# Kernel optimization log

Measured on AMD Instinct MI355X. Metric: run time of the kernel, lower is better.

Reference implementation:

```python
import jax, jax.numpy as jnp
import numpy as np

N, T, D, H = 64, 1024, 512, 512

def setup_inputs() -> dict:
    key = jax.random.key(0)
    k1, k2, k3, k4 = jax.random.split(key, 4)
    x = jax.random.normal(k1, (N, T, D), dtype=jnp.float32)
    h0 = jax.random.normal(k2, (N, H), dtype=jnp.float32)
    Wx = jax.random.normal(k3, (D, H), dtype=jnp.float32) / jnp.sqrt(jnp.float32(D))
    Wh = jax.random.normal(k4, (H, H), dtype=jnp.float32) / jnp.sqrt(jnp.float32(H))
    b = jnp.zeros((H,), dtype=jnp.float32)
    return {"x": x, "h0": h0, "Wx": Wx, "Wh": Wh, "b": b}

def reference(x, h0, Wx, Wh, b):
    # Precompute input projection for all timesteps: (N,T,H)
    xW = jnp.einsum('ntd,dh->nth', x, Wx) + b
    # Sequential recurrence over time via lax.scan
    def step(prev_h, xw_t):
        next_h = jnp.tanh(prev_h @ Wh + xw_t)  # (N,H)
        return next_h, next_h
    # scan over time axis: move T to leading axis
    _, h_seq = jax.lax.scan(step, h0, jnp.swapaxes(xW, 0, 1))  # (T,N,H)
    return jnp.swapaxes(h_seq, 0, 1)  # (N,T,H)
```

## Files before the change

### kernel.cpp

```cpp
#include <hip/hip_runtime.h>
#include <hip/hip_fp16.h>
#include <cstddef>
#include <cstdint>

#define NB 64
#define TT 1024
#define DD 512
#define HH 512

typedef _Float16 h2_t __attribute__((ext_vector_type(2)));
typedef __attribute__((ext_vector_type(8))) short bf16x8;
typedef __attribute__((ext_vector_type(4))) float f32x4;
typedef __attribute__((ext_vector_type(8))) unsigned short ushort8;

__device__ __forceinline__ float dot2f(uint32_t a, uint32_t b, float c) {
#if __has_builtin(__builtin_amdgcn_fdot2)
    return __builtin_amdgcn_fdot2(__builtin_bit_cast(h2_t, a),
                                  __builtin_bit_cast(h2_t, b), c, false);
#else
    __half2 av = __builtin_bit_cast(__half2, a);
    __half2 bv = __builtin_bit_cast(__half2, b);
    float2 af = __half22float2(av), bf = __half22float2(bv);
    return fmaf(af.x, bf.x, fmaf(af.y, bf.y, c));
#endif
}

__device__ __forceinline__ float fast_tanh(float z) {
    z = fmaxf(-15.f, fminf(15.f, z));
    float u = __builtin_amdgcn_exp2f(-2.885390082f * z);
    return (1.f - u) * __builtin_amdgcn_rcpf(1.f + u);
}

__device__ __forceinline__ unsigned short f2bf(float f) {
    uint32_t u = __builtin_bit_cast(uint32_t, f);
    u += 0x7FFFu + ((u >> 16) & 1u);
    return (unsigned short)(u >> 16);
}

__global__ void conv_wt(const float* __restrict__ W,
                        unsigned short* __restrict__ Wt) {
    int n = blockIdx.x;
    int kc = threadIdx.x;
    ushort8 o;
#pragma unroll
    for (int i = 0; i < 8; ++i)
        o[i] = f2bf(W[(size_t)(kc * 8 + i) * HH + n]);
    *reinterpret_cast<ushort8*>(&Wt[(size_t)n * DD + kc * 8]) = o;
}

#define GBM 128
#define GBN 128
#define GBK 64
#define LDSW 72

__global__ __launch_bounds__(256, 4) void gemm_bf16f(
    const float* __restrict__ X,
    const unsigned short* __restrict__ Bt,
    const float* __restrict__ bias,
    float* __restrict__ C)
{
    __shared__ unsigned short As[GBM * LDSW];
    __shared__ unsigned short Bs[GBN * LDSW];

    const int tid  = threadIdx.x;
    const int m0   = blockIdx.x * GBM;
    const int n0   = blockIdx.y * GBN;
    const int lane = tid & 63;
    const int wave = tid >> 6;
    const int wm   = wave >> 1;
    const int wn   = wave & 1;

    const int axr = tid >> 1;
    const int axc = (tid & 1) * 32;
    const int srow = tid >> 3;
    const int sch  = tid & 7;

    f32x4 acc[4][4] = {};

    const int arow = wm * 64 + (lane & 15);
    const int brow = wn * 64 + (lane & 15);
    const int koff = (lane >> 4) * 8;

    for (int kt = 0; kt < DD / GBK; ++kt) {
        const int k0 = kt * GBK;
        {
            const float* xp = &X[(size_t)(m0 + axr) * DD + k0 + axc];
#pragma unroll
            for (int i = 0; i < 4; ++i) {
                float4 a = *reinterpret_cast<const float4*>(&xp[i * 8]);
                float4 b = *reinterpret_cast<const float4*>(&xp[i * 8 + 4]);
                ushort8 o;
                o[0] = f2bf(a.x); o[1] = f2bf(a.y);
                o[2] = f2bf(a.z); o[3] = f2bf(a.w);
                o[4] = f2bf(b.x); o[5] = f2bf(b.y);
                o[6] = f2bf(b.z); o[7] = f2bf(b.w);
                *reinterpret_cast<ushort8*>(&As[axr * LDSW + axc + i * 8]) = o;
            }
        }
#pragma unroll
        for (int p = 0; p < 4; ++p) {
            const int row = srow + p * 32;
            *reinterpret_cast<ushort8*>(&Bs[row * LDSW + sch * 8]) =
                *reinterpret_cast<const ushort8*>(
                    &Bt[(size_t)(n0 + row) * DD + k0 + sch * 8]);
        }
        __syncthreads();

#pragma unroll
        for (int kk = 0; kk < GBK; kk += 32) {
            bf16x8 af[4], bf[4];
#pragma unroll
            for (int mt = 0; mt < 4; ++mt)
                af[mt] = *reinterpret_cast<const bf16x8*>(
                    &As[(arow + mt * 16) * LDSW + kk + koff]);
#pragma unroll
            for (int nt = 0; nt < 4; ++nt)
                bf[nt] = *reinterpret_cast<const bf16x8*>(
                    &Bs[(brow + nt * 16) * LDSW + kk + koff]);
#pragma unroll
            for (int mt = 0; mt < 4; ++mt)
#pragma unroll
                for (int nt = 0; nt < 4; ++nt)
                    acc[mt][nt] = __builtin_amdgcn_mfma_f32_16x16x32_bf16(
                        af[mt], bf[nt], acc[mt][nt], 0, 0, 0);
        }
        __syncthreads();
    }

#pragma unroll
    for (int nt = 0; nt < 4; ++nt) {
        const int col = n0 + wn * 64 + nt * 16 + (lane & 15);
        const float bv = bias[col];
#pragma unroll
        for (int mt = 0; mt < 4; ++mt) {
            const int rbase = m0 + wm * 64 + mt * 16 + (lane >> 4) * 4;
#pragma unroll
            for (int r = 0; r < 4; ++r)
                C[(size_t)(rbase + r) * HH + col] = acc[mt][nt][r] + bv;
        }
    }
}

#define BM 128
#define BN 128
#define BK 8

__global__ __launch_bounds__(256, 2) void gemm_xw(
    const float* __restrict__ A,
    const float* __restrict__ B,
    const float* __restrict__ bias,
    float* __restrict__ C)
{
    __shared__ float As[BK][BM];
    __shared__ float Bs[BK][BN];

    const int tid  = threadIdx.x;
    const int tm   = tid >> 4;
    const int tn   = tid & 15;
    const int row0 = blockIdx.x * BM;
    const int col0 = blockIdx.y * BN;

    const int ar = tid >> 1;
    const int ac = (tid & 1) * 4;
    const int br = tid >> 5;
    const int bc = (tid & 31) * 4;

    float acc[8][8];
#pragma unroll
    for (int i = 0; i < 8; ++i)
#pragma unroll
        for (int j = 0; j < 8; ++j) acc[i][j] = 0.f;

    for (int k0 = 0; k0 < DD; k0 += BK) {
        float4 av = *reinterpret_cast<const float4*>(
            &A[(size_t)(row0 + ar) * DD + k0 + ac]);
        float4 bv = *reinterpret_cast<const float4*>(
            &B[(size_t)(k0 + br) * HH + col0 + bc]);

        As[ac + 0][ar] = av.x;
        As[ac + 1][ar] = av.y;
        As[ac + 2][ar] = av.z;
        As[ac + 3][ar] = av.w;
        *reinterpret_cast<float4*>(&Bs[br][bc]) = bv;
        __syncthreads();

#pragma unroll
        for (int kk = 0; kk < BK; ++kk) {
            float a[8], b[8];
            *reinterpret_cast<float4*>(&a[0]) =
                *reinterpret_cast<const float4*>(&As[kk][tm * 8]);
            *reinterpret_cast<float4*>(&a[4]) =
                *reinterpret_cast<const float4*>(&As[kk][tm * 8 + 4]);
            *reinterpret_cast<float4*>(&b[0]) =
                *reinterpret_cast<const float4*>(&Bs[kk][tn * 8]);
            *reinterpret_cast<float4*>(&b[4]) =
                *reinterpret_cast<const float4*>(&Bs[kk][tn * 8 + 4]);
#pragma unroll
            for (int i = 0; i < 8; ++i)
#pragma unroll
                for (int j = 0; j < 8; ++j)
                    acc[i][j] = fmaf(a[i], b[j], acc[i][j]);
        }
        __syncthreads();
    }

#pragma unroll
    for (int i = 0; i < 8; ++i) {
        const int row = row0 + tm * 8 + i;
#pragma unroll
        for (int j = 0; j < 8; j += 4) {
            const int col = col0 + tn * 8 + j;
            float4 o;
            o.x = acc[i][j + 0] + bias[col + 0];
            o.y = acc[i][j + 1] + bias[col + 1];
            o.z = acc[i][j + 2] + bias[col + 2];
            o.w = acc[i][j + 3] + bias[col + 3];
            *reinterpret_cast<float4*>(&C[(size_t)row * HH + col]) = o;
        }
    }
}

__global__ __launch_bounds__(1024, 4) void rnn_scan_pk2(
    const float* __restrict__ Wh,
    const float* __restrict__ h0,
    float* __restrict__ out,
    uint64_t* __restrict__ truth,
    uint64_t* __restrict__ mirror,
    int* __restrict__ meta)
{
    __shared__ __align__(16) uint32_t hp[2][HH / 2];
    __shared__ float partial[16][128];
    __shared__ int sh_batch, sh_role, sh_fast;

    const int tid = threadIdx.x;

    int xcd_raw;
    asm volatile("s_getreg_b32 %0, hwreg(HW_REG_XCC_ID)" : "=s"(xcd_raw));
    const int xcd = xcd_raw & 7;

    if (tid == 0) {
        int pos = __hip_atomic_fetch_add(&meta[xcd], 1, __ATOMIC_RELAXED,
                                         __HIP_MEMORY_SCOPE_AGENT);
        __hip_atomic_fetch_add(&meta[8], 1, __ATOMIC_RELEASE,
                               __HIP_MEMORY_SCOPE_AGENT);
        while (__hip_atomic_load(&meta[8], __ATOMIC_ACQUIRE,
                                 __HIP_MEMORY_SCOPE_AGENT) < 256)
            __builtin_amdgcn_s_sleep(8);
        int c[8];
#pragma unroll
        for (int q = 0; q < 8; ++q)
            c[q] = __hip_atomic_load(&meta[q], __ATOMIC_RELAXED,
                                     __HIP_MEMORY_SCOPE_AGENT);
        int totalfull = 0, basefull = 0, rembase = 0;
#pragma unroll
        for (int q = 0; q < 8; ++q) totalfull += c[q] >> 2;
        for (int q = 0; q < xcd; ++q) {
            basefull += c[q] >> 2;
            rembase  += c[q] & 3;
        }
        const int nf4 = (c[xcd] >> 2) << 2;
        if (pos < nf4) {
            sh_batch = basefull + (pos >> 2);
            sh_role  = pos & 3;
            sh_fast  = 1;
        } else {
            int ridx = rembase + (pos - nf4);
            sh_batch = totalfull + (ridx >> 2);
            sh_role  = ridx & 3;
            sh_fast  = 0;
        }
    }
    __syncthreads();

    const int n    = sh_batch;
    const int jb   = sh_role << 7;
    const int pb   = sh_role << 6;
    const int fast = sh_fast;

    const int w = tid >> 6;
    const int l = tid & 63;

    uint32_t w0[16], w1[16];
    {
        const float* wc = Wh + (size_t)(w * 32) * HH + jb + l;
#pragma unroll
        for (int p = 0; p < 16; ++p) {
            float e0 = wc[(size_t)(2 * p) * HH];
            float e1 = wc[(size_t)(2 * p + 1) * HH];
            w0[p] = __builtin_bit_cast(uint32_t, __floats2half2_rn(e0, e1));
            float f0 = wc[(size_t)(2 * p) * HH + 64];
            float f1 = wc[(size_t)(2 * p + 1) * HH + 64];
            w1[p] = __builtin_bit_cast(uint32_t, __floats2half2_rn(f0, f1));
        }
    }

    if (tid < HH)
        ((__half*)hp[0])[tid] = __float2half(h0[(size_t)n * HH + tid]);
    __syncthreads();

    float* outn = out + (size_t)n * TT * HH;
    uint64_t* tru = truth  + (size_t)n * 2 * 256;
    uint64_t* mir = mirror + (size_t)n * 2 * 256;

    const int ppi = (pb + 64 + (tid - 64)) & 255;

    int cur = 0;
    for (int t = 0; t < TT; ++t) {
        const uint32_t T = (uint32_t)(t + 1);
        const int slot = (int)(T & 1u);

        float2 xw2 = {0.f, 0.f};
        if (tid < 64)
            xw2 = *reinterpret_cast<const float2*>(
                &outn[(size_t)t * HH + jb + 2 * tid]);

        const uint32_t* hpw = &hp[cur][w * 16];
        float a0 = 0.f, a1 = 0.f, b0 = 0.f, b1 = 0.f;
#pragma unroll
        for (int q = 0; q < 4; ++q) {
            uint4 hv = ((const uint4*)hpw)[q];
            a0 = dot2f(hv.x, w0[4 * q + 0], a0);
            b0 = dot2f(hv.x, w1[4 * q + 0], b0);
            a1 = dot2f(hv.y, w0[4 * q + 1], a1);
            b1 = dot2f(hv.y, w1[4 * q + 1], b1);
            a0 = dot2f(hv.z, w0[4 * q + 2], a0);
            b0 = dot2f(hv.z, w1[4 * q + 2], b0);
            a1 = dot2f(hv.w, w0[4 * q + 3], a1);
            b1 = dot2f(hv.w, w1[4 * q + 3], b1);
        }
        partial[w][l] = a0 + a1;
        partial[w][64 + l] = b0 + b1;
        __syncthreads();

        uint32_t* hpn32 = hp[cur ^ 1];
        if (tid < 64) {
            float s0 = 0.f, s1 = 0.f;
#pragma unroll
            for (int ww = 0; ww < 16; ++ww) {
                float2 pv = *reinterpret_cast<const float2*>(
                    &partial[ww][2 * tid]);
                s0 += pv.x; s1 += pv.y;
            }
            float hh0 = fast_tanh(s0 + xw2.x);
            float hh1 = fast_tanh(s1 + xw2.y);
            uint32_t ph = __builtin_bit_cast(uint32_t,
                                             __floats2half2_rn(hh0, hh1));
            uint64_t pk = ((uint64_t)T << 32) | ph;
            const int idx = slot * 256 + pb + tid;
            if (fast) {
                asm volatile("global_atomic_swap_x2 %0, %1, off"
                             :: "v"((uint64_t)&mir[idx]), "v"(pk) : "memory");
            } else {
                __hip_atomic_store(&tru[idx], pk, __ATOMIC_RELAXED,
                                   __HIP_MEMORY_SCOPE_AGENT);
            }
            float2 ov; ov.x = hh0; ov.y = hh1;
            *reinterpret_cast<float2*>(
                &outn[(size_t)t * HH + jb + 2 * tid]) = ov;
            hpn32[pb + tid] = ph;
        } else if (tid < 256) {
            const int idx = slot * 256 + ppi;
            uint64_t v;
            if (fast) {
                const uint64_t maddr = (uint64_t)&mir[idx];
                const uint64_t zero = 0;
                while (true) {
                    asm volatile(
                        "global_atomic_add_x2 %0, %1, %2, off sc0\n\t"
                        "s_waitcnt vmcnt(0)"
                        : "=v"(v) : "v"(maddr), "v"(zero) : "memory");
                    if ((uint32_t)(v >> 32) == T) break;
                    __builtin_amdgcn_s_sleep(1);
                }
            } else {
                v = __hip_atomic_load(&tru[idx], __ATOMIC_RELAXED,
                                      __HIP_MEMORY_SCOPE_AGENT);
                while ((uint32_t)(v >> 32) != T) {
                    __builtin_amdgcn_s_sleep(1);
                    v = __hip_atomic_load(&tru[idx], __ATOMIC_RELAXED,
                                          __HIP_MEMORY_SCOPE_AGENT);
                }
            }
            hpn32[ppi] = (uint32_t)v;
        }
        __syncthreads();
        cur ^= 1;
    }
}

__global__ __launch_bounds__(512, 2) void rnn_scan_f32(
    const float* __restrict__ Wh,
    const float* __restrict__ h0,
    float* __restrict__ out)
{
    __shared__ float hbuf[2][HH];
    const int n = blockIdx.x;
    const int j = threadIdx.x;

    hbuf[0][j] = h0[(size_t)n * HH + j];
    __syncthreads();

    float* outn = out + (size_t)n * TT * HH;
    const float* __restrict__ wp = Wh + j;

    int cur = 0;
    for (int t = 0; t < TT; ++t) {
        float acc = outn[(size_t)t * HH + j];
        const float* hc = hbuf[cur];
#pragma unroll 4
        for (int k = 0; k < HH; k += 4) {
            float4 hv = *reinterpret_cast<const float4*>(&hc[k]);
            acc = fmaf(hv.x, wp[(size_t)(k + 0) * HH], acc);
            acc = fmaf(hv.y, wp[(size_t)(k + 1) * HH], acc);
            acc = fmaf(hv.z, wp[(size_t)(k + 2) * HH], acc);
            acc = fmaf(hv.w, wp[(size_t)(k + 3) * HH], acc);
        }
        float hn = tanhf(acc);
        outn[(size_t)t * HH + j] = hn;
        hbuf[cur ^ 1][j] = hn;
        cur ^= 1;
        __syncthreads();
    }
}

extern "C" void kernel_launch(void* const* d_in, const int* in_sizes, int n_in,
                              void* d_out, int out_size, void* d_ws, size_t ws_size,
                              hipStream_t stream) {
    const float* x  = (const float*)d_in[0];
    const float* h0 = (const float*)d_in[1];
    const float* Wx = (const float*)d_in[2];
    const float* Wh = (const float*)d_in[3];
    const float* b  = (const float*)d_in[4];
    float* out = (float*)d_out;

    const long   M      = (long)NB * TT;
    const size_t pkt_b  = (size_t)NB * 2 * 256 * 8;
    const size_t meta_b = 4096;
    const size_t wt_b   = (size_t)HH * DD * 2;

    const size_t off_mir  = pkt_b;
    const size_t off_meta = 2 * pkt_b;
    const size_t off_wt   = 2 * pkt_b + meta_b;
    const size_t need_all = off_wt + wt_b;
    const size_t need_mid = 2 * pkt_b + meta_b;

    if (ws_size >= need_all) {
        uint64_t*       truth  = (uint64_t*)d_ws;
        uint64_t*       mirror = (uint64_t*)((char*)d_ws + off_mir);
        int*            meta   = (int*)((char*)d_ws + off_meta);
        unsigned short* Wt     = (unsigned short*)((char*)d_ws + off_wt);

        conv_wt<<<HH, 64, 0, stream>>>(Wx, Wt);
        dim3 gg(M / GBM, HH / GBN);
        gemm_bf16f<<<gg, 256, 0, stream>>>(x, Wt, b, out);
        hipMemsetAsync(meta, 0, 64, stream);
        rnn_scan_pk2<<<256, 1024, 0, stream>>>(Wh, h0, out, truth, mirror, meta);
    } else if (ws_size >= need_mid) {
        uint64_t* truth  = (uint64_t*)d_ws;
        uint64_t* mirror = (uint64_t*)((char*)d_ws + off_mir);
        int*      meta   = (int*)((char*)d_ws + off_meta);
        dim3 g1(M / BM, HH / BN);
        gemm_xw<<<g1, 256, 0, stream>>>(x, Wx, b, out);
        hipMemsetAsync(meta, 0, 64, stream);
        rnn_scan_pk2<<<256, 1024, 0, stream>>>(Wh, h0, out, truth, mirror, meta);
    } else {
        dim3 g1(M / BM, HH / BN);
        gemm_xw<<<g1, 256, 0, stream>>>(x, Wx, b, out);
        rnn_scan_f32<<<NB, 512, 0, stream>>>(Wh, h0, out);
    }
}
```

Baseline: 1.542 ms.

## Replace XCD-aware dynamic block mapping with static blockIdx mapping in RNN scan

Removes the startup grid-wide rendezvous, in which blocks atomically counted per-XCD arrivals and then computed batch and role assignments, along with the memset launch that cleared that metadata. Batch and role now come straight from blockIdx (n = blk & 63, r = blk >> 6). This relies on round-robin XCD dispatch to keep the four blocks of a batch on the same XCD. The exchange now always publishes with an atomic swap and polls with plain agent-scope atomic loads, with no sleep in the spin loop. The risks are that co-location now depends on how the hardware dispatches blocks, and that spinning without sleep adds memory traffic.

```diff
diff --git a/kernel.cpp b/kernel.cpp
--- a/kernel.cpp
+++ b/kernel.cpp
@@ -220,63 +220,22 @@
     }
 }
 
-__global__ __launch_bounds__(1024, 4) void rnn_scan_pk2(
+__global__ __launch_bounds__(1024, 4) void rnn_scan_fin(
     const float* __restrict__ Wh,
     const float* __restrict__ h0,
     float* __restrict__ out,
-    uint64_t* __restrict__ truth,
-    uint64_t* __restrict__ mirror,
-    int* __restrict__ meta)
+    uint64_t* __restrict__ exch)
 {
     __shared__ __align__(16) uint32_t hp[2][HH / 2];
     __shared__ float partial[16][128];
-    __shared__ int sh_batch, sh_role, sh_fast;
+
+    const int blk = blockIdx.x;
+    const int n   = blk & 63;
+    const int r   = blk >> 6;
+    const int jb  = r << 7;
+    const int pb  = r << 6;
 
     const int tid = threadIdx.x;
-
-    int xcd_raw;
-    asm volatile("s_getreg_b32 %0, hwreg(HW_REG_XCC_ID)" : "=s"(xcd_raw));
-    const int xcd = xcd_raw & 7;
-
-    if (tid == 0) {
-        int pos = __hip_atomic_fetch_add(&meta[xcd], 1, __ATOMIC_RELAXED,
-                                         __HIP_MEMORY_SCOPE_AGENT);
-        __hip_atomic_fetch_add(&meta[8], 1, __ATOMIC_RELEASE,
-                               __HIP_MEMORY_SCOPE_AGENT);
-        while (__hip_atomic_load(&meta[8], __ATOMIC_ACQUIRE,
-                                 __HIP_MEMORY_SCOPE_AGENT) < 256)
-            __builtin_amdgcn_s_sleep(8);
-        int c[8];
-#pragma unroll
-        for (int q = 0; q < 8; ++q)
-            c[q] = __hip_atomic_load(&meta[q], __ATOMIC_RELAXED,
-                                     __HIP_MEMORY_SCOPE_AGENT);
-        int totalfull = 0, basefull = 0, rembase = 0;
-#pragma unroll
-        for (int q = 0; q < 8; ++q) totalfull += c[q] >> 2;
-        for (int q = 0; q < xcd; ++q) {
-            basefull += c[q] >> 2;
-            rembase  += c[q] & 3;
-        }
-        const int nf4 = (c[xcd] >> 2) << 2;
-        if (pos < nf4) {
-            sh_batch = basefull + (pos >> 2);
-            sh_role  = pos & 3;
-            sh_fast  = 1;
-        } else {
-            int ridx = rembase + (pos - nf4);
-            sh_batch = totalfull + (ridx >> 2);
-            sh_role  = ridx & 3;
-            sh_fast  = 0;
-        }
-    }
-    __syncthreads();
-
-    const int n    = sh_batch;
-    const int jb   = sh_role << 7;
-    const int pb   = sh_role << 6;
-    const int fast = sh_fast;
-
     const int w = tid >> 6;
     const int l = tid & 63;
 
@@ -299,8 +258,7 @@
     __syncthreads();
 
     float* outn = out + (size_t)n * TT * HH;
-    uint64_t* tru = truth  + (size_t)n * 2 * 256;
-    uint64_t* mir = mirror + (size_t)n * 2 * 256;
+    uint64_t* ex = exch + (size_t)n * 2 * 256;
 
     const int ppi = (pb + 64 + (tid - 64)) & 255;
 
@@ -347,39 +305,19 @@
                                              __floats2half2_rn(hh0, hh1));
             uint64_t pk = ((uint64_t)T << 32) | ph;
             const int idx = slot * 256 + pb + tid;
-            if (fast) {
-                asm volatile("global_atomic_swap_x2 %0, %1, off"
-                             :: "v"((uint64_t)&mir[idx]), "v"(pk) : "memory");
-            } else {
-                __hip_atomic_store(&tru[idx], pk, __ATOMIC_RELAXED,
-                                   __HIP_MEMORY_SCOPE_AGENT);
-            }
+            asm volatile("global_atomic_swap_x2 %0, %1, off"
+                         :: "v"((uint64_t)&ex[idx]), "v"(pk) : "memory");
             float2 ov; ov.x = hh0; ov.y = hh1;
             *reinterpret_cast<float2*>(
                 &outn[(size_t)t * HH + jb + 2 * tid]) = ov;
             hpn32[pb + tid] = ph;
         } else if (tid < 256) {
             const int idx = slot * 256 + ppi;
-            uint64_t v;
-            if (fast) {
-                const uint64_t maddr = (uint64_t)&mir[idx];
-                const uint64_t zero = 0;
-                while (true) {
-                    asm volatile(
-                        "global_atomic_add_x2 %0, %1, %2, off sc0\n\t"
-                        "s_waitcnt vmcnt(0)"
-                        : "=v"(v) : "v"(maddr), "v"(zero) : "memory");
-                    if ((uint32_t)(v >> 32) == T) break;
-                    __builtin_amdgcn_s_sleep(1);
-                }
-            } else {
-                v = __hip_atomic_load(&tru[idx], __ATOMIC_RELAXED,
+            uint64_t v = __hip_atomic_load(&ex[idx], __ATOMIC_RELAXED,
+                                           __HIP_MEMORY_SCOPE_AGENT);
+            while ((uint32_t)(v >> 32) != T) {
+                v = __hip_atomic_load(&ex[idx], __ATOMIC_RELAXED,
                                       __HIP_MEMORY_SCOPE_AGENT);
-                while ((uint32_t)(v >> 32) != T) {
-                    __builtin_amdgcn_s_sleep(1);
-                    v = __hip_atomic_load(&tru[idx], __ATOMIC_RELAXED,
-                                          __HIP_MEMORY_SCOPE_AGENT);
-                }
             }
             hpn32[ppi] = (uint32_t)v;
         }
@@ -435,34 +373,23 @@
 
     const long   M      = (long)NB * TT;
     const size_t pkt_b  = (size_t)NB * 2 * 256 * 8;
-    const size_t meta_b = 4096;
     const size_t wt_b   = (size_t)HH * DD * 2;
-
-    const size_t off_mir  = pkt_b;
-    const size_t off_meta = 2 * pkt_b;
-    const size_t off_wt   = 2 * pkt_b + meta_b;
-    const size_t need_all = off_wt + wt_b;
-    const size_t need_mid = 2 * pkt_b + meta_b;
+    const size_t need_all = pkt_b + wt_b;
+    const size_t need_mid = pkt_b;
 
     if (ws_size >= need_all) {
-        uint64_t*       truth  = (uint64_t*)d_ws;
-        uint64_t*       mirror = (uint64_t*)((char*)d_ws + off_mir);
-        int*            meta   = (int*)((char*)d_ws + off_meta);
-        unsigned short* Wt     = (unsigned short*)((char*)d_ws + off_wt);
+        uint64_t*       exch = (uint64_t*)d_ws;
+        unsigned short* Wt   = (unsigned short*)((char*)d_ws + pkt_b);
 
         conv_wt<<<HH, 64, 0, stream>>>(Wx, Wt);
         dim3 gg(M / GBM, HH / GBN);
         gemm_bf16f<<<gg, 256, 0, stream>>>(x, Wt, b, out);
-        hipMemsetAsync(meta, 0, 64, stream);
-        rnn_scan_pk2<<<256, 1024, 0, stream>>>(Wh, h0, out, truth, mirror, meta);
+        rnn_scan_fin<<<256, 1024, 0, stream>>>(Wh, h0, out, exch);
     } else if (ws_size >= need_mid) {
-        uint64_t* truth  = (uint64_t*)d_ws;
-        uint64_t* mirror = (uint64_t*)((char*)d_ws + off_mir);
-        int*      meta   = (int*)((char*)d_ws + off_meta);
+        uint64_t* exch = (uint64_t*)d_ws;
         dim3 g1(M / BM, HH / BN);
         gemm_xw<<<g1, 256, 0, stream>>>(x, Wx, b, out);
-        hipMemsetAsync(meta, 0, 64, stream);
-        rnn_scan_pk2<<<256, 1024, 0, stream>>>(Wh, h0, out, truth, mirror, meta);
+        rnn_scan_fin<<<256, 1024, 0, stream>>>(Wh, h0, out, exch);
     } else {
         dim3 g1(M / BM, HH / BN);
         gemm_xw<<<g1, 256, 0, stream>>>(x, Wx, b, out);
```

Result: faster. 1.491 ms (-3.3%).
